# Optimization experiments

Measured on AMD Instinct MI355X. Metric: run time of the kernel, lower is better.

## Reference

```python
import jax, jax.numpy as jnp
import numpy as np

B = 4096          # batch_size * world_size
D = 256           # embedding dim
TEMP = 0.5        # temperature
EPS = 1e-8


def setup_inputs() -> dict:
    key = jax.random.key(0)
    k1, k2 = jax.random.split(key)
    z_i = jax.random.normal(k1, (B, D), dtype=jnp.float32)
    z_j = jax.random.normal(k2, (B, D), dtype=jnp.float32)
    return {"z_i": z_i, "z_j": z_j}


def reference(z_i, z_j):
    N = 2 * B
    z = jnp.concatenate([z_i, z_j], axis=0)                      # [N, D]
    # cosine similarity = normalized dot products (normalize + GEMM)
    norm = jnp.sqrt(jnp.sum(z * z, axis=-1, keepdims=True))
    zn = z / jnp.maximum(norm, EPS)
    sim = (zn @ zn.T) / TEMP                                     # [N, N]
    # positives: pairs (i, i+B) and (i+B, i)
    idx = jnp.arange(N)
    pos = sim[idx, (idx + B) % N]                                # [N]
    # CE with label 0 over [pos, negatives]; the candidate set equals the
    # full sim row minus the diagonal (pos is re-included), so:
    sim_masked = jnp.where(jnp.eye(N, dtype=bool), -jnp.inf, sim)
    lse = jax.nn.logsumexp(sim_masked, axis=1)                   # [N]
    loss = jnp.sum(lse - pos) / N                                # reduction='sum' then /N
    return loss
```

## Files before the change

### kernel.cpp

```cpp
#include <hip/hip_runtime.h>
#include <hip/hip_bf16.h>
#include <cmath>

#define B_SZ 4096
#define N_SZ 8192
#define D_SZ 256
#define EPS 1e-8f
#define EXPC 0.01127105500694503f
#define EXPB -2.8853900817779268f

typedef __attribute__((ext_vector_type(4))) float f32x4;
typedef __attribute__((ext_vector_type(4))) int   i32x4;
typedef __attribute__((ext_vector_type(8))) int   i32x8;

__device__ __forceinline__ void dma16(const void* g, void* l) {
    __builtin_amdgcn_global_load_lds(
        (const __attribute__((address_space(1))) unsigned int*)g,
        (__attribute__((address_space(3))) unsigned int*)l, 16, 0, 0);
}


__global__ __launch_bounds__(256) void prep_kernel(const float* __restrict__ zi,
                                                   const float* __restrict__ zj,
                                                   char* __restrict__ znb,
                                                   float* __restrict__ pos,
                                                   float* __restrict__ accf,
                                                   unsigned* __restrict__ counter) {
    if (blockIdx.x == 0 && threadIdx.x == 0) { *accf = 0.0f; *counter = 0u; }
    const int wave = threadIdx.x >> 6, lane = threadIdx.x & 63;
    const int i = blockIdx.x * 4 + wave;
    float4 a = reinterpret_cast<const float4*>(zi + (size_t)i * D_SZ)[lane];
    float4 b = reinterpret_cast<const float4*>(zj + (size_t)i * D_SZ)[lane];
    float ssa = a.x * a.x + a.y * a.y + a.z * a.z + a.w * a.w;
    float ssb = b.x * b.x + b.y * b.y + b.z * b.z + b.w * b.w;
    float dab = a.x * b.x + a.y * b.y + a.z * b.z + a.w * b.w;
    #pragma unroll
    for (int off = 32; off; off >>= 1) {
        ssa += __shfl_xor(ssa, off, 64);
        ssb += __shfl_xor(ssb, off, 64);
        dab += __shfl_xor(dab, off, 64);
    }
    const float invna = 1.0f / fmaxf(sqrtf(ssa), EPS);
    const float invnb = 1.0f / fmaxf(sqrtf(ssb), EPS);
    if (lane == 0) {
        float p = dab * invna * invnb * 2.0f;
        pos[i] = p;
        pos[i + B_SZ] = p;
    }
    const float sa = invna * 16.0f, sb = invnb * 16.0f;
    const int koff = (lane >> 2) * 1024 + (lane & 3) * 4;
    {
        int pk = __builtin_amdgcn_cvt_pk_fp8_f32(a.x * sa, a.y * sa, 0, false);
        pk     = __builtin_amdgcn_cvt_pk_fp8_f32(a.z * sa, a.w * sa, pk, true);
        *reinterpret_cast<int*>(znb + (size_t)(i >> 6) * 16384 + koff + (i & 63) * 16) = pk;
    }
    {
        const int r = i + B_SZ;
        int pk = __builtin_amdgcn_cvt_pk_fp8_f32(b.x * sb, b.y * sb, 0, false);
        pk     = __builtin_amdgcn_cvt_pk_fp8_f32(b.z * sb, b.w * sb, pk, true);
        *reinterpret_cast<int*>(znb + (size_t)(r >> 6) * 16384 + koff + (r & 63) * 16) = pk;
    }
}

__global__ __launch_bounds__(256, 3) void simlse_kernel(const char* __restrict__ znb,
                                                        float* __restrict__ partial) {
    __shared__ __attribute__((aligned(16))) char blds[32768];
    __shared__ float cs[4][256];

    const int t = threadIdx.x;
    const int wave = t >> 6, lane = t & 63;

    int rt, chunk;
    {
        const int x = blockIdx.x & 7;
        int j = blockIdx.x >> 3;
        int p = x;
        if (j >= 33) { j -= 33; p = x + 8; }
        if (j <= p) { rt = j; chunk = p; }
        else        { rt = j - (p + 1); chunk = 31 - p; }
    }
    const bool offdiag = (rt != chunk);

    const int rl = lane & 15;
    const int kg = lane >> 4;
    const int i0 = rt * 256 + wave * 64;

    #define STAGE(H)                                                              \
        {                                                                         \
            const char* gp = znb + (size_t)chunk * 65536 + (H) * 32768 + t * 16;  \
            char* lp = blds + t * 16;                                             \
            _Pragma("unroll")                                                     \
            for (int c = 0; c < 8; ++c) dma16(gp + c * 4096, lp + c * 4096);      \
        }

    STAGE(0);

    const char* ap = znb + (size_t)(rt * 4 + wave) * 16384 + rl * 16;
    i32x8 afrag[4][2];
    #pragma unroll
    for (int g = 0; g < 4; ++g)
        #pragma unroll
        for (int kc = 0; kc < 2; ++kc) {
            i32x4 lo = *reinterpret_cast<const i32x4*>(
                ap + (kc * 8 + kg * 2) * 1024 + g * 256);
            i32x4 hi = *reinterpret_cast<const i32x4*>(
                ap + (kc * 8 + kg * 2 + 1) * 1024 + g * 256);
            afrag[g][kc] = __builtin_shufflevector(lo, hi, 0, 1, 2, 3, 4, 5, 6, 7);
        }

    float s_acc[4][4];
    #pragma unroll
    for (int g = 0; g < 4; ++g)
        #pragma unroll
        for (int r = 0; r < 4; ++r) s_acc[g][r] = 0.0f;

    const char* bp0 = blds + kg * 2048 + rl * 16;

    i32x8 bf0, bf1;
    f32x4 accA[4], accB[4];

    #define LOADB(FL)                                                             \
        {                                                                         \
            const char* bq = bp0 + ((FL) >> 2) * 16384 + ((FL) & 3) * 256;        \
            i32x4 l0 = *reinterpret_cast<const i32x4*>(bq);                       \
            i32x4 l1 = *reinterpret_cast<const i32x4*>(bq + 1024);                \
            i32x4 l2 = *reinterpret_cast<const i32x4*>(bq + 8192);                \
            i32x4 l3 = *reinterpret_cast<const i32x4*>(bq + 9216);                \
            bf0 = __builtin_shufflevector(l0, l1, 0, 1, 2, 3, 4, 5, 6, 7);        \
            bf1 = __builtin_shufflevector(l2, l3, 0, 1, 2, 3, 4, 5, 6, 7);        \
        }

    #define MFMA8(ACC)                                                            \
        {                                                                         \
            _Pragma("unroll")                                                     \
            for (int g = 0; g < 4; ++g) ACC[g] = (f32x4){0.f, 0.f, 0.f, 0.f};     \
            _Pragma("unroll")                                                     \
            for (int g = 0; g < 4; ++g)                                           \
                asm("v_mfma_f32_16x16x128_f8f6f4 %0, %1, %2, %0"                  \
                    : "+v"(ACC[g]) : "v"(afrag[g][0]), "v"(bf0));                 \
            _Pragma("unroll")                                                     \
            for (int g = 0; g < 4; ++g)                                           \
                asm("v_mfma_f32_16x16x128_f8f6f4 %0, %1, %2, %0"                  \
                    : "+v"(ACC[g]) : "v"(afrag[g][1]), "v"(bf1));                 \
        }

    #define EXPSUM(ACC, F)                                                        \
        {                                                                         \
            float cthr = 0.0f;                                                    \
            _Pragma("unroll")                                                     \
            for (int g = 0; g < 4; ++g)                                           \
                _Pragma("unroll")                                                 \
                for (int r = 0; r < 4; ++r) {                                     \
                    float e = __builtin_amdgcn_exp2f(fmaf(ACC[g][r], EXPC, EXPB)); \
                    s_acc[g][r] += e;                                             \
                    cthr += e;                                                    \
                }                                                                 \
            cthr += __shfl_xor(cthr, 16, 64);                                     \
            cthr += __shfl_xor(cthr, 32, 64);                                     \
            if (offdiag && lane < 16)                                             \
                cs[wave][(F) * 16 + rl] = cthr;                                   \
        }

    __syncthreads();

    LOADB(0); MFMA8(accA);
    #pragma unroll 1
    for (int fo = 0; fo < 3; ++fo) {
        const int f1 = 2 * fo + 1, f2 = 2 * fo + 2;
        LOADB(f1); MFMA8(accB);
        asm volatile("s_nop 7");
        EXPSUM(accA, f1 - 1);
        LOADB(f2); MFMA8(accA);
        asm volatile("s_nop 7");
        EXPSUM(accB, f2 - 1);
    }
    LOADB(7); MFMA8(accB);
    asm volatile("s_nop 7");
    EXPSUM(accA, 6);

    __syncthreads();
    STAGE(1);
    EXPSUM(accB, 7);
    __syncthreads();

    LOADB(0); MFMA8(accA);
    #pragma unroll 1
    for (int fo = 0; fo < 3; ++fo) {
        const int f1 = 2 * fo + 1, f2 = 2 * fo + 2;
        LOADB(f1); MFMA8(accB);
        asm volatile("s_nop 7");
        EXPSUM(accA, 8 + f1 - 1);
        LOADB(f2); MFMA8(accA);
        asm volatile("s_nop 7");
        EXPSUM(accB, 8 + f2 - 1);
    }
    LOADB(7); MFMA8(accB);
    asm volatile("s_nop 7");
    EXPSUM(accA, 14);
    asm volatile("s_nop 7");
    EXPSUM(accB, 15);

    #pragma unroll
    for (int g = 0; g < 4; ++g)
        #pragma unroll
        for (int r = 0; r < 4; ++r) {
            float v = s_acc[g][r];
            #pragma unroll
            for (int off = 1; off < 16; off <<= 1) v += __shfl_xor(v, off, 64);
            if (rl == 0)
                partial[chunk * N_SZ + i0 + g * 16 + kg * 4 + r] = v;
        }

    if (offdiag) {
        __syncthreads();
        float v = cs[0][t] + cs[1][t] + cs[2][t] + cs[3][t];
        partial[rt * N_SZ + chunk * 256 + t] = v;
    }
    #undef STAGE
    #undef LOADB
    #undef MFMA8
    #undef EXPSUM
}

__global__ __launch_bounds__(256) void rowsum_kernel(const float* __restrict__ partial,
                                                     const float* __restrict__ pos,
                                                     float* __restrict__ accf,
                                                     unsigned* __restrict__ counter,
                                                     float* __restrict__ out) {
    const int row = blockIdx.x * 256 + threadIdx.x;
    float s = -1.0f;
    #pragma unroll
    for (int c = 0; c < 32; ++c) s += partial[c * N_SZ + row];
    float acc = 2.0f + logf(s) - pos[row];
    #pragma unroll
    for (int off = 32; off; off >>= 1) acc += __shfl_xor(acc, off, 64);
    __shared__ float w[4];
    if ((threadIdx.x & 63) == 0) w[threadIdx.x >> 6] = acc;
    __syncthreads();
    if (threadIdx.x == 0) {
        atomicAdd(accf, w[0] + w[1] + w[2] + w[3]);
        __threadfence();
        unsigned old = atomicAdd(counter, 1u);
        if (old == 31u) {
            float tot = atomicAdd(accf, 0.0f);
            out[0] = tot / (float)N_SZ;
        }
    }
}

extern "C" void kernel_launch(void* const* d_in, const int* in_sizes, int n_in,
                              void* d_out, int out_size, void* d_ws, size_t ws_size,
                              hipStream_t stream) {
    const float* zi = (const float*)d_in[0];
    const float* zj = (const float*)d_in[1];

    char* ws = (char*)d_ws;
    char* znb       = ws;
    float* pos      = (float*)(ws + 2097152);
    float* partial  = (float*)(ws + 2097152 + 32768);
    float* accf     = (float*)(ws + 2097152 + 32768 + 1048576);
    unsigned* counter = (unsigned*)(ws + 2097152 + 32768 + 1048576 + 4);
    float* out = (float*)d_out;

    prep_kernel<<<B_SZ / 4, 256, 0, stream>>>(zi, zj, znb, pos, accf, counter);
    simlse_kernel<<<528, 256, 0, stream>>>(znb, partial);
    rowsum_kernel<<<32, 256, 0, stream>>>(partial, pos, accf, counter, out);
}
```

Before: 31.73 us.

## Split symmetric sim tiles into 256x128 blocks and raise MFMA priority

Each block of the symmetric similarity/LSE kernel now covers a 256-row by 128-column tile instead of 256x256, doubling the grid to 1056 blocks. This drops the second LDS staging phase and its barriers, and gives the GPU more blocks for load balance. Row and column partial sums go to two separate partial buffers, and the final row-sum kernel reads a variable number of partials per row tile. s_setprio is also raised around the MFMA sequences. In exchange, each A fragment is reused over half as many columns and per-block launch and epilogue overhead doubles.

```diff
diff --git a/kernel.cpp b/kernel.cpp
--- a/kernel.cpp
+++ b/kernel.cpp
@@ -63,37 +63,34 @@
 }
 
 __global__ __launch_bounds__(256, 3) void simlse_kernel(const char* __restrict__ znb,
-                                                        float* __restrict__ partial) {
+                                                        float* __restrict__ partial1,
+                                                        float* __restrict__ partial2) {
     __shared__ __attribute__((aligned(16))) char blds[32768];
-    __shared__ float cs[4][256];
+    __shared__ float cs[4][128];
 
     const int t = threadIdx.x;
     const int wave = t >> 6, lane = t & 63;
 
-    int rt, chunk;
-    {
-        const int x = blockIdx.x & 7;
-        int j = blockIdx.x >> 3;
-        int p = x;
-        if (j >= 33) { j -= 33; p = x + 8; }
-        if (j <= p) { rt = j; chunk = p; }
-        else        { rt = j - (p + 1); chunk = 31 - p; }
-    }
-    const bool offdiag = (rt != chunk);
+    int bid = blockIdx.x, rt = 0;
+    #pragma unroll 1
+    for (; rt < 32; ++rt) {
+        int cnt = 64 - 2 * rt;
+        if (bid < cnt) break;
+        bid -= cnt;
+    }
+    const int c2 = 2 * rt + bid;
+    const bool offdiag = ((c2 >> 1) != rt);
 
     const int rl = lane & 15;
     const int kg = lane >> 4;
     const int i0 = rt * 256 + wave * 64;
 
-    #define STAGE(H)                                                              \
-        {                                                                         \
-            const char* gp = znb + (size_t)chunk * 65536 + (H) * 32768 + t * 16;  \
-            char* lp = blds + t * 16;                                             \
-            _Pragma("unroll")                                                     \
-            for (int c = 0; c < 8; ++c) dma16(gp + c * 4096, lp + c * 4096);      \
-        }
-
-    STAGE(0);
+    {
+        const char* gp = znb + (size_t)c2 * 32768 + t * 16;
+        char* lp = blds + t * 16;
+        #pragma unroll
+        for (int c = 0; c < 8; ++c) dma16(gp + c * 4096, lp + c * 4096);
+    }
 
     const char* ap = znb + (size_t)(rt * 4 + wave) * 16384 + rl * 16;
     i32x8 afrag[4][2];
@@ -119,9 +116,9 @@
     i32x8 bf0, bf1;
     f32x4 accA[4], accB[4];
 
-    #define LOADB(FL)                                                             \
+    #define LOADB(F)                                                              \
         {                                                                         \
-            const char* bq = bp0 + ((FL) >> 2) * 16384 + ((FL) & 3) * 256;        \
+            const char* bq = bp0 + ((F) >> 2) * 16384 + ((F) & 3) * 256;          \
             i32x4 l0 = *reinterpret_cast<const i32x4*>(bq);                       \
             i32x4 l1 = *reinterpret_cast<const i32x4*>(bq + 1024);                \
             i32x4 l2 = *reinterpret_cast<const i32x4*>(bq + 8192);                \
@@ -134,6 +131,7 @@
         {                                                                         \
             _Pragma("unroll")                                                     \
             for (int g = 0; g < 4; ++g) ACC[g] = (f32x4){0.f, 0.f, 0.f, 0.f};     \
+            __builtin_amdgcn_s_setprio(1);                                        \
             _Pragma("unroll")                                                     \
             for (int g = 0; g < 4; ++g)                                           \
                 asm("v_mfma_f32_16x16x128_f8f6f4 %0, %1, %2, %0"                  \
@@ -142,6 +140,7 @@
             for (int g = 0; g < 4; ++g)                                           \
                 asm("v_mfma_f32_16x16x128_f8f6f4 %0, %1, %2, %0"                  \
                     : "+v"(ACC[g]) : "v"(afrag[g][1]), "v"(bf1));                 \
+            __builtin_amdgcn_s_setprio(0);                                        \
         }
 
     #define EXPSUM(ACC, F)                                                        \
@@ -177,28 +176,8 @@
     LOADB(7); MFMA8(accB);
     asm volatile("s_nop 7");
     EXPSUM(accA, 6);
-
-    __syncthreads();
-    STAGE(1);
+    asm volatile("s_nop 7");
     EXPSUM(accB, 7);
-    __syncthreads();
-
-    LOADB(0); MFMA8(accA);
-    #pragma unroll 1
-    for (int fo = 0; fo < 3; ++fo) {
-        const int f1 = 2 * fo + 1, f2 = 2 * fo + 2;
-        LOADB(f1); MFMA8(accB);
-        asm volatile("s_nop 7");
-        EXPSUM(accA, 8 + f1 - 1);
-        LOADB(f2); MFMA8(accA);
-        asm volatile("s_nop 7");
-        EXPSUM(accB, 8 + f2 - 1);
-    }
-    LOADB(7); MFMA8(accB);
-    asm volatile("s_nop 7");
-    EXPSUM(accA, 14);
-    asm volatile("s_nop 7");
-    EXPSUM(accB, 15);
 
     #pragma unroll
     for (int g = 0; g < 4; ++g)
@@ -208,29 +187,34 @@
             #pragma unroll
             for (int off = 1; off < 16; off <<= 1) v += __shfl_xor(v, off, 64);
             if (rl == 0)
-                partial[chunk * N_SZ + i0 + g * 16 + kg * 4 + r] = v;
+                partial1[(size_t)c2 * N_SZ + i0 + g * 16 + kg * 4 + r] = v;
         }
 
     if (offdiag) {
         __syncthreads();
-        float v = cs[0][t] + cs[1][t] + cs[2][t] + cs[3][t];
-        partial[rt * N_SZ + chunk * 256 + t] = v;
-    }
-    #undef STAGE
+        if (t < 128) {
+            float v = cs[0][t] + cs[1][t] + cs[2][t] + cs[3][t];
+            partial2[(size_t)rt * N_SZ + c2 * 128 + t] = v;
+        }
+    }
     #undef LOADB
     #undef MFMA8
     #undef EXPSUM
 }
 
-__global__ __launch_bounds__(256) void rowsum_kernel(const float* __restrict__ partial,
+__global__ __launch_bounds__(256) void rowsum_kernel(const float* __restrict__ partial1,
+                                                     const float* __restrict__ partial2,
                                                      const float* __restrict__ pos,
                                                      float* __restrict__ accf,
                                                      unsigned* __restrict__ counter,
                                                      float* __restrict__ out) {
-    const int row = blockIdx.x * 256 + threadIdx.x;
+    const int T = blockIdx.x;
+    const int row = T * 256 + threadIdx.x;
     float s = -1.0f;
-    #pragma unroll
-    for (int c = 0; c < 32; ++c) s += partial[c * N_SZ + row];
+    #pragma unroll 1
+    for (int c2 = 2 * T; c2 < 64; ++c2) s += partial1[(size_t)c2 * N_SZ + row];
+    #pragma unroll 1
+    for (int r = 0; r < T; ++r) s += partial2[(size_t)r * N_SZ + row];
     float acc = 2.0f + logf(s) - pos[row];
     #pragma unroll
     for (int off = 32; off; off >>= 1) acc += __shfl_xor(acc, off, 64);
@@ -257,12 +241,13 @@
     char* ws = (char*)d_ws;
     char* znb       = ws;
     float* pos      = (float*)(ws + 2097152);
-    float* partial  = (float*)(ws + 2097152 + 32768);
-    float* accf     = (float*)(ws + 2097152 + 32768 + 1048576);
-    unsigned* counter = (unsigned*)(ws + 2097152 + 32768 + 1048576 + 4);
+    float* partial1 = (float*)(ws + 2097152 + 32768);
+    float* partial2 = (float*)(ws + 2097152 + 32768 + 2097152);
+    float* accf     = (float*)(ws + 2097152 + 32768 + 2097152 + 1048576);
+    unsigned* counter = (unsigned*)(ws + 2097152 + 32768 + 2097152 + 1048576 + 4);
     float* out = (float*)d_out;
 
     prep_kernel<<<B_SZ / 4, 256, 0, stream>>>(zi, zj, znb, pos, accf, counter);
-    simlse_kernel<<<528, 256, 0, stream>>>(znb, partial);
-    rowsum_kernel<<<32, 256, 0, stream>>>(partial, pos, accf, counter, out);
-}
+    simlse_kernel<<<1056, 256, 0, stream>>>(znb, partial1, partial2);
+    rowsum_kernel<<<32, 256, 0, stream>>>(partial1, partial2, pos, accf, counter, out);
+}
```

After: 46.88 us. 1.48x slower.
